# Performance work log

Measured on AMD Instinct MI355X. Metric: run time of the kernel, lower is better.

Reference implementation:

```python
import jax, jax.numpy as jnp
import numpy as np

B, N, D, W, IMG = 16384, 20, 64, 64, 2048
NUM_USERS, NUM_ITEMS, NUM_INGRE = 100000, 201000, 33001


def setup_inputs() -> dict:
    key = jax.random.key(0)
    ks = jax.random.split(key, 24)
    s = lambda *sh: 1.0 / np.sqrt(sh[0])
    inp = {
        'user_input': jax.random.randint(ks[0], (B,), 0, NUM_USERS),
        'item_input': jax.random.randint(ks[1], (B,), 0, NUM_ITEMS),
        'ingre_input': jax.random.randint(ks[2], (B, N), 0, NUM_INGRE),
        'image_input': jax.random.normal(ks[3], (B, IMG), dtype=jnp.float32),
        'ingre_num': jax.random.randint(ks[4], (B,), 1, N + 1),
        'user_emb': jax.random.normal(ks[5], (NUM_USERS, D), dtype=jnp.float32) * 0.01,
        'item_emb': jax.random.normal(ks[6], (NUM_ITEMS, D), dtype=jnp.float32) * 0.01,
        'ingre_emb': jax.random.normal(ks[7], (NUM_INGRE, D), dtype=jnp.float32) * 0.01,
        'W_image_w': jax.random.normal(ks[8], (IMG, D), dtype=jnp.float32) * s(IMG),
        'W_image_b': jnp.zeros((D,), jnp.float32),
        'b_image': jnp.zeros((1, D), jnp.float32),
        'W_concat_w': jax.random.normal(ks[9], (3 * D, D), dtype=jnp.float32) * s(3 * D),
        'W_concat_b': jnp.zeros((D,), jnp.float32),
        'b_concat': jnp.zeros((1, D), jnp.float32),
        'h_w': jax.random.normal(ks[10], (D, 1), dtype=jnp.float32) * s(D),
        'h_b': jnp.zeros((1,), jnp.float32),
        'W_att_ingre_w': jax.random.normal(ks[11], (3 * D, W), dtype=jnp.float32) * s(3 * D),
        'W_att_ingre_b': jnp.zeros((W,), jnp.float32),
        'b_att_ingre': jnp.zeros((1, W), jnp.float32),
        'v': jnp.ones((W, 1), jnp.float32),
        'W_att_com_w': jax.random.normal(ks[12], (2 * D, W), dtype=jnp.float32) * s(2 * D),
        'W_att_com_b': jnp.zeros((W,), jnp.float32),
        'b_att_com': jnp.zeros((1, W), jnp.float32),
        'v_c': jnp.ones((W, 1), jnp.float32),
    }
    return inp


def reference(user_input, item_input, ingre_input, image_input, ingre_num,
              user_emb, item_emb, ingre_emb,
              W_image_w, W_image_b, b_image,
              W_concat_w, W_concat_b, b_concat, h_w, h_b,
              W_att_ingre_w, W_att_ingre_b, b_att_ingre, v,
              W_att_com_w, W_att_com_b, b_att_com, v_c):
    b = user_input.shape[0]
    ue = user_emb[user_input]                       # [B, D]
    ie = item_emb[item_input]                       # [B, D]
    qe = ingre_emb[ingre_input]                     # [B, N, D]
    img = image_input @ W_image_w + W_image_b + b_image  # [B, D]

    # ---- ingredient-level attention ----
    n = qe.shape[1]
    tile_p = jnp.broadcast_to(ue[:, None, :], (b, n, ue.shape[-1]))
    tile_i = jnp.broadcast_to(img[:, None, :], (b, n, img.shape[-1]))
    concat_v = jnp.concatenate([qe, tile_p, tile_i], axis=2)     # [B, N, 3D]
    mlp = jnp.tanh(concat_v @ W_att_ingre_w + W_att_ingre_b + b_att_ingre[0])  # [B, N, W]
    A_ = (mlp @ v)[..., 0]                                        # [B, N]
    mask = (jnp.arange(n)[None, :] < ingre_num[:, None]).astype(A_.dtype)
    A_ = A_ * mask + (1.0 - mask) * (-1e12)
    A = jax.nn.softmax(A_, axis=1)[..., None]                     # [B, N, 1]
    ingre_att = jnp.sum(A * qe, axis=1)                           # [B, D]

    # ---- component-level attention (faithful to original cat+view order) ----
    cp = jnp.concatenate([
        jnp.concatenate([ue, ie], axis=1),
        jnp.concatenate([ue, ingre_att], axis=1),
        jnp.concatenate([ue, img], axis=1),
    ], axis=0)                                                    # [3B, 2D]
    ch = jnp.tanh(cp @ W_att_com_w + W_att_com_b + b_att_com[0])  # [3B, W]
    scores = (ch @ v_c).reshape(b, -1)                            # [B, 3] (row-major, as torch .view)
    Bw = jax.nn.softmax(scores, axis=1)[..., None]                # [B, 3, 1]
    ce = jnp.stack([ie, ingre_att, img], axis=1)                  # [B, 3, D]
    item_att = jnp.sum(Bw * ce, axis=1)                           # [B, D]

    # ---- prediction head ----
    uic = jnp.concatenate([ue, item_att, ue * item_att], axis=-1) # [B, 3D]
    hidden = jax.nn.relu(uic @ W_concat_w + W_concat_b + b_concat[0])
    out = hidden @ h_w + h_b                                      # [B, 1]
    return out
```

## Files before the change

kernel.cpp:

```cpp
#include <hip/hip_runtime.h>
#include <hip/hip_fp16.h>

#define BB 16384
#define NN 20
#define DD 64
#define IMGK 2048

using bf16x8 = __attribute__((ext_vector_type(8))) short;
using f32x4  = __attribute__((ext_vector_type(4))) float;

typedef __attribute__((address_space(1))) const unsigned int GUint;
typedef __attribute__((address_space(3))) unsigned int LUint;
__device__ __forceinline__ void gl_lds16(const void* g, void* l) {
  __builtin_amdgcn_global_load_lds((GUint*)g, (LUint*)l, 16, 0, 0);
}

__device__ __forceinline__ float waveReduceSum(float x) {
#pragma unroll
  for (int off = 32; off > 0; off >>= 1) x += __shfl_xor(x, off, 64);
  return x;
}

__device__ __forceinline__ float fast_tanh(float x) {
  float e = __expf(2.f * x);
  return 1.f - __fdividef(2.f, e + 1.f);
}

__device__ __forceinline__ short f2bf(float f) {
  union { float f; unsigned u; } c; c.f = f;
  unsigned r = c.u + 0x7fffu + ((c.u >> 16) & 1u);
  return (short)(r >> 16);
}
__device__ __forceinline__ float bf2f(short s) {
  union { unsigned u; float f; } c; c.u = ((unsigned)(unsigned short)s) << 16;
  return c.f;
}

__device__ __forceinline__ unsigned pack_hi(float a, float b) {
  unsigned ua = __float_as_uint(a), ub = __float_as_uint(b);
  return (ub & 0xffff0000u) | (ua >> 16);
}
__device__ __forceinline__ float trunc_bf(float a) {
  return __uint_as_float(__float_as_uint(a) & 0xffff0000u);
}

__global__ __launch_bounds__(256)
void prep_kernel(const float* __restrict__ Wimg, const float* __restrict__ W1,
                 short* __restrict__ Wf, short* __restrict__ W1f) {
  int i = blockIdx.x * 256 + threadIdx.x;
  if (i < 32768) {
    const int lane = i & 63;
    const int h = (i >> 6) & 1;
    const int tt = (i >> 7) & 3;
    const int ks = (i >> 9) & 1;
    const int kq = i >> 10;
    const int n = 16 * tt + (lane & 15);
    const int kb = kq * 64 + ks * 32 + (lane >> 4) * 8;
    union { short s[8]; bf16x8 v; } o;
#pragma unroll
    for (int j = 0; j < 8; ++j) {
      float f = Wimg[(size_t)(kb + j) * 64 + n];
      short hi = f2bf(f);
      o.s[j] = h == 0 ? hi : f2bf(f - bf2f(hi));
    }
    reinterpret_cast<bf16x8*>(Wf)[i] = o.v;
  } else if (i < 32768 + 1536) {
    const int j = i - 32768;
    const int lane = j & 63;
    const int wt = (j >> 6) & 3;
    const int ks = j >> 8;
    const int n = 16 * wt + (lane & 15);
    const int kb = ks * 32 + (lane >> 4) * 8;
    union { short s[8]; bf16x8 v; } o;
#pragma unroll
    for (int jj = 0; jj < 8; ++jj)
      o.s[jj] = f2bf(W1[(size_t)(kb + jj) * 64 + n]);
    reinterpret_cast<bf16x8*>(W1f)[j] = o.v;
  }
}

__global__ __launch_bounds__(256, 5)
void img_gemm_mfma(const float* __restrict__ img_in,
                   const short* __restrict__ Wf,
                   __half* __restrict__ pp) {
  __shared__ short wlds[8192];
  __shared__ float alds[4096];
  const int t = threadIdx.x;
  const int wave = t >> 6, lane = t & 63;
  const int lr = lane & 15, lk = lane >> 4;
  const int kq = blockIdx.x & 31, rgb = blockIdx.x >> 5;
  const int r0 = rgb * 64;
  __half* pout = pp + (size_t)kq * BB * 64;

  const short* wsrc = Wf + (size_t)kq * 8192;
#pragma unroll
  for (int i = 0; i < 4; ++i) {
    int j = i * 256 + t;
    gl_lds16(wsrc + j * 8, wlds + j * 8);
  }
#pragma unroll
  for (int i = 0; i < 4; ++i) {
    int j = i * 256 + t;
    int r = j >> 4, c = j & 15;
    int gc = (c ^ (r & 7)) * 4;
    gl_lds16(img_in + (size_t)(r0 + r) * IMGK + kq * 64 + gc, alds + j * 4);
  }
  asm volatile("s_waitcnt vmcnt(0)" ::: "memory");
  __syncthreads();

  const int arow = wave * 16 + lr;
  const int rx = arow & 7;
  float4 Af[2][2];
#pragma unroll
  for (int ks = 0; ks < 2; ++ks) {
    const int s0 = ks * 8 + lk * 2;
    Af[ks][0] = *reinterpret_cast<const float4*>(alds + arow * 64 + (s0 ^ rx) * 4);
    Af[ks][1] = *reinterpret_cast<const float4*>(alds + arow * 64 + ((s0 + 1) ^ rx) * 4);
  }
  const bf16x8* wp = reinterpret_cast<const bf16x8*>(wlds);
  f32x4 aHH[4], aER[4];
#pragma unroll
  for (int tt = 0; tt < 4; ++tt) {
    aHH[tt] = (f32x4){0.f, 0.f, 0.f, 0.f};
    aER[tt] = (f32x4){0.f, 0.f, 0.f, 0.f};
  }
#pragma unroll
  for (int ks = 0; ks < 2; ++ks) {
    float4 va = Af[ks][0], vb = Af[ks][1];
    union { unsigned u[4]; bf16x8 v; } hi, lo;
    hi.u[0] = pack_hi(va.x, va.y);
    hi.u[1] = pack_hi(va.z, va.w);
    hi.u[2] = pack_hi(vb.x, vb.y);
    hi.u[3] = pack_hi(vb.z, vb.w);
    lo.u[0] = pack_hi(va.x - trunc_bf(va.x), va.y - trunc_bf(va.y));
    lo.u[1] = pack_hi(va.z - trunc_bf(va.z), va.w - trunc_bf(va.w));
    lo.u[2] = pack_hi(vb.x - trunc_bf(vb.x), vb.y - trunc_bf(vb.y));
    lo.u[3] = pack_hi(vb.z - trunc_bf(vb.z), vb.w - trunc_bf(vb.w));
#pragma unroll
    for (int tt = 0; tt < 4; ++tt) {
      bf16x8 wh = wp[((ks * 4 + tt) * 2 + 0) * 64 + lane];
      bf16x8 wl = wp[((ks * 4 + tt) * 2 + 1) * 64 + lane];
      aHH[tt] = __builtin_amdgcn_mfma_f32_16x16x32_bf16(hi.v, wh, aHH[tt], 0, 0, 0);
      aER[tt] = __builtin_amdgcn_mfma_f32_16x16x32_bf16(hi.v, wl, aER[tt], 0, 0, 0);
      aER[tt] = __builtin_amdgcn_mfma_f32_16x16x32_bf16(lo.v, wh, aER[tt], 0, 0, 0);
    }
  }
#pragma unroll
  for (int tt = 0; tt < 4; ++tt)
#pragma unroll
    for (int r = 0; r < 4; ++r)
      pout[(size_t)(r0 + wave * 16 + 4 * lk + r) * 64 + 16 * tt + lr] =
          __float2half(aHH[tt][r] + aER[tt][r]);
}

__global__ __launch_bounds__(256, 3)
void mid_kernel(const int* __restrict__ user_input,
                const int* __restrict__ ingre_input,
                const int* __restrict__ ingre_num,
                const float* __restrict__ user_emb,
                const float* __restrict__ ingre_emb,
                const __half* __restrict__ pp,
                const float* __restrict__ Wb, const float* __restrict__ bimg,
                const short* __restrict__ W1f,
                const float* __restrict__ Wib, const float* __restrict__ bai,
                const float* __restrict__ v,
                float* __restrict__ ws_img,
                float* __restrict__ ws_ia) {
  __shared__ short wflds[12288];
  __shared__ short qe_s[4][32][88];
  __shared__ short ui_s[4][128];
  __shared__ float sc_s[4][32];
  const int t = threadIdx.x;
  const int wave = t >> 6, lane = t & 63;
  const int lr = lane & 15, lk = lane >> 4;
  const int b = blockIdx.x * 4 + wave;

  for (int i = t; i < 1536; i += 256)
    reinterpret_cast<bf16x8*>(wflds)[i] = reinterpret_cast<const bf16x8*>(W1f)[i];

  float qv[NN];
#pragma unroll
  for (int n = 0; n < NN; ++n) {
    const int gi = ingre_input[b * NN + n];
    qv[n] = ingre_emb[(size_t)gi * 64 + lane];
  }
  float s = Wb[lane] + bimg[lane];
#pragma unroll
  for (int kq = 0; kq < 32; ++kq)
    s += __half2float(pp[(size_t)kq * BB * 64 + (size_t)b * 64 + lane]);
  const int u = user_input[b];
  const float ue = user_emb[(size_t)u * 64 + lane];
  ws_img[(size_t)b * 64 + lane] = s;
  float vv[4], biasw[4];
#pragma unroll
  for (int wt = 0; wt < 4; ++wt) {
    vv[wt] = v[16 * wt + lr];
    biasw[wt] = Wib[16 * wt + lr] + bai[16 * wt + lr];
  }

#pragma unroll
  for (int n = 0; n < NN; ++n) qe_s[wave][n][lane] = f2bf(qv[n]);
#pragma unroll
  for (int n = NN; n < 32; ++n) qe_s[wave][n][lane] = 0;
  ui_s[wave][lane] = f2bf(ue);
  ui_s[wave][64 + lane] = f2bf(s);
  __syncthreads();

  bf16x8 aq0[2], aq1[2], au[4];
#pragma unroll
  for (int ks = 0; ks < 2; ++ks) {
    aq0[ks] = *reinterpret_cast<const bf16x8*>(&qe_s[wave][lr][ks * 32 + lk * 8]);
    aq1[ks] = *reinterpret_cast<const bf16x8*>(&qe_s[wave][16 + lr][ks * 32 + lk * 8]);
  }
#pragma unroll
  for (int ks = 0; ks < 4; ++ks)
    au[ks] = *reinterpret_cast<const bf16x8*>(&ui_s[wave][ks * 32 + lk * 8]);

  const bf16x8* wp = reinterpret_cast<const bf16x8*>(wflds);
  f32x4 accq[2][4], accb[4];
#pragma unroll
  for (int wt = 0; wt < 4; ++wt) {
    accq[0][wt] = (f32x4){0.f, 0.f, 0.f, 0.f};
    accq[1][wt] = (f32x4){0.f, 0.f, 0.f, 0.f};
    accb[wt] = (f32x4){0.f, 0.f, 0.f, 0.f};
  }
#pragma unroll
  for (int ks = 0; ks < 2; ++ks)
#pragma unroll
    for (int wt = 0; wt < 4; ++wt) {
      bf16x8 w = wp[(ks * 4 + wt) * 64 + lane];
      accq[0][wt] = __builtin_amdgcn_mfma_f32_16x16x32_bf16(aq0[ks], w, accq[0][wt], 0, 0, 0);
      accq[1][wt] = __builtin_amdgcn_mfma_f32_16x16x32_bf16(aq1[ks], w, accq[1][wt], 0, 0, 0);
    }
#pragma unroll
  for (int ks = 2; ks < 6; ++ks)
#pragma unroll
    for (int wt = 0; wt < 4; ++wt) {
      bf16x8 w = wp[(ks * 4 + wt) * 64 + lane];
      accb[wt] = __builtin_amdgcn_mfma_f32_16x16x32_bf16(au[ks - 2], w, accb[wt], 0, 0, 0);
    }
  float basew[4];
#pragma unroll
  for (int wt = 0; wt < 4; ++wt) basew[wt] = accb[wt][0] + biasw[wt];

  float sp[2][4];
#pragma unroll
  for (int nt = 0; nt < 2; ++nt)
#pragma unroll
    for (int r = 0; r < 4; ++r) {
      float sv = 0.f;
#pragma unroll
      for (int wt = 0; wt < 4; ++wt) {
        float x = accq[nt][wt][r] + basew[wt];
        sv = fmaf(fast_tanh(x), vv[wt], sv);
      }
      sp[nt][r] = sv;
    }
#pragma unroll
  for (int off = 1; off < 16; off <<= 1)
#pragma unroll
    for (int nt = 0; nt < 2; ++nt)
#pragma unroll
      for (int r = 0; r < 4; ++r) sp[nt][r] += __shfl_xor(sp[nt][r], off, 64);
  if (lr == 0) {
#pragma unroll
    for (int r = 0; r < 4; ++r) {
      sc_s[wave][4 * lk + r] = sp[0][r];
      sc_s[wave][16 + 4 * lk + r] = sp[1][r];
    }
  }
  asm volatile("s_waitcnt lgkmcnt(0)" ::: "memory");
  float scn[NN];
#pragma unroll
  for (int q = 0; q < 5; ++q) {
    float4 s4 = *reinterpret_cast<const float4*>(&sc_s[wave][4 * q]);
    scn[4 * q + 0] = s4.x; scn[4 * q + 1] = s4.y;
    scn[4 * q + 2] = s4.z; scn[4 * q + 3] = s4.w;
  }
  asm volatile("s_waitcnt lgkmcnt(0)" ::: "memory");
  const int num = ingre_num[b];
  float m = -3e38f;
#pragma unroll
  for (int n = 0; n < NN; ++n) {
    scn[n] = (n < num) ? scn[n] : -1e12f;
    m = fmaxf(m, scn[n]);
  }
  float ssum = 0.f;
#pragma unroll
  for (int n = 0; n < NN; ++n) {
    scn[n] = __expf(scn[n] - m);
    ssum += scn[n];
  }
  const float inv = __fdividef(1.f, ssum);
  float ia = 0.f;
#pragma unroll
  for (int n = 0; n < NN; ++n) ia = fmaf(scn[n], qv[n], ia);
  ws_ia[(size_t)b * 64 + lane] = ia * inv;
}

__global__ __launch_bounds__(256, 4)
void com_score_kernel(const int* __restrict__ user_input,
                      const int* __restrict__ item_input,
                      const float* __restrict__ user_emb,
                      const float* __restrict__ item_emb,
                      const float* __restrict__ Wc,
                      const float* __restrict__ Wcb,
                      const float* __restrict__ bat,
                      const float* __restrict__ vc,
                      const float* __restrict__ ws_img,
                      const float* __restrict__ ws_ia,
                      float* __restrict__ ws_flat) {
  __shared__ float Wclds[128 * 64];
  __shared__ float x_s[4][4][64];
  const int t = threadIdx.x;
  for (int i = t; i < 128 * 64 / 4; i += 256)
    reinterpret_cast<float4*>(Wclds)[i] = reinterpret_cast<const float4*>(Wc)[i];
  __syncthreads();
  const int wave = t >> 6, lane = t & 63;
  const float bb = Wcb[lane] + bat[lane];
  const float vcl = vc[lane];
  const int b0 = blockIdx.x * 16 + wave * 4;
#pragma unroll 1
  for (int bi = 0; bi < 4; ++bi) {
    const int b = b0 + bi;
    const int u = user_input[b];
    const int it = item_input[b];
    x_s[wave][0][lane] = user_emb[(size_t)u * 64 + lane];
    x_s[wave][1][lane] = item_emb[(size_t)it * 64 + lane];
    x_s[wave][2][lane] = ws_ia[(size_t)b * 64 + lane];
    x_s[wave][3][lane] = ws_img[(size_t)b * 64 + lane];
    asm volatile("s_waitcnt lgkmcnt(0)" ::: "memory");
    const float4* u4 = reinterpret_cast<const float4*>(&x_s[wave][0][0]);
    float up = 0.f;
#pragma unroll
    for (int d0 = 0; d0 < 16; ++d0) {
      float4 q = u4[d0];
      int d = d0 * 4;
      up = fmaf(q.x, Wclds[(d + 0) * 64 + lane],
           fmaf(q.y, Wclds[(d + 1) * 64 + lane],
           fmaf(q.z, Wclds[(d + 2) * 64 + lane],
           fmaf(q.w, Wclds[(d + 3) * 64 + lane], up))));
    }
    float sc[3];
#pragma unroll
    for (int c = 0; c < 3; ++c) {
      const float4* y4 = reinterpret_cast<const float4*>(&x_s[wave][1 + c][0]);
      float s = bb + up;
#pragma unroll
      for (int d0 = 0; d0 < 16; ++d0) {
        float4 q = y4[d0];
        int d = 64 + d0 * 4;
        s = fmaf(q.x, Wclds[(d + 0) * 64 + lane],
            fmaf(q.y, Wclds[(d + 1) * 64 + lane],
            fmaf(q.z, Wclds[(d + 2) * 64 + lane],
            fmaf(q.w, Wclds[(d + 3) * 64 + lane], s))));
      }
      sc[c] = waveReduceSum(fast_tanh(s) * vcl);
    }
    if (lane == 0) {
      ws_flat[b] = sc[0];
      ws_flat[BB + b] = sc[1];
      ws_flat[2 * BB + b] = sc[2];
    }
    asm volatile("s_waitcnt lgkmcnt(0)" ::: "memory");
  }
}

__global__ __launch_bounds__(256, 3)
void head_kernel(const int* __restrict__ user_input,
                 const int* __restrict__ item_input,
                 const float* __restrict__ user_emb,
                 const float* __restrict__ item_emb,
                 const float* __restrict__ Wcat,
                 const float* __restrict__ Wcatb,
                 const float* __restrict__ bcat,
                 const float* __restrict__ hw,
                 const float* __restrict__ hb,
                 const float* __restrict__ ws_img,
                 const float* __restrict__ ws_ia,
                 const float* __restrict__ ws_flat,
                 float* __restrict__ out) {
  __shared__ float Wlds[192 * 64];
  __shared__ float ue_s[4][64];
  __shared__ float itt_s[4][64];
  const int t = threadIdx.x;
  for (int i = t; i < 192 * 64 / 4; i += 256)
    reinterpret_cast<float4*>(Wlds)[i] = reinterpret_cast<const float4*>(Wcat)[i];
  __syncthreads();
  const int wave = t >> 6, lane = t & 63;
  const float bb = Wcatb[lane] + bcat[lane];
  const float hwl = hw[lane];
  const float hbv = hb[0];
  const int b0 = blockIdx.x * 16 + wave * 4;
#pragma unroll 1
  for (int bi = 0; bi < 4; ++bi) {
    const int b = b0 + bi;
    const float s0 = ws_flat[3 * b + 0];
    const float s1 = ws_flat[3 * b + 1];
    const float s2 = ws_flat[3 * b + 2];
    const float m = fmaxf(s0, fmaxf(s1, s2));
    const float e0 = __expf(s0 - m), e1 = __expf(s1 - m), e2 = __expf(s2 - m);
    const float inv = 1.0f / (e0 + e1 + e2);
    const int u = user_input[b];
    const int it = item_input[b];
    const float uev = user_emb[(size_t)u * 64 + lane];
    const float itt = (e0 * item_emb[(size_t)it * 64 + lane] +
                       e1 * ws_ia[(size_t)b * 64 + lane] +
                       e2 * ws_img[(size_t)b * 64 + lane]) * inv;
    ue_s[wave][lane] = uev;
    itt_s[wave][lane] = itt;
    asm volatile("s_waitcnt lgkmcnt(0)" ::: "memory");
    const float4* u4 = reinterpret_cast<const float4*>(&ue_s[wave][0]);
    const float4* i4 = reinterpret_cast<const float4*>(&itt_s[wave][0]);
    float h = bb;
#pragma unroll
    for (int d0 = 0; d0 < 16; ++d0) {
      float4 uu = u4[d0];
      float4 ii = i4[d0];
      int d = d0 * 4;
      h = fmaf(uu.x, Wlds[(d + 0) * 64 + lane], h);
      h = fmaf(ii.x, Wlds[(64 + d + 0) * 64 + lane], h);
      h = fmaf(uu.x * ii.x, Wlds[(128 + d + 0) * 64 + lane], h);
      h = fmaf(uu.y, Wlds[(d + 1) * 64 + lane], h);
      h = fmaf(ii.y, Wlds[(64 + d + 1) * 64 + lane], h);
      h = fmaf(uu.y * ii.y, Wlds[(128 + d + 1) * 64 + lane], h);
      h = fmaf(uu.z, Wlds[(d + 2) * 64 + lane], h);
      h = fmaf(ii.z, Wlds[(64 + d + 2) * 64 + lane], h);
      h = fmaf(uu.z * ii.z, Wlds[(128 + d + 2) * 64 + lane], h);
      h = fmaf(uu.w, Wlds[(d + 3) * 64 + lane], h);
      h = fmaf(ii.w, Wlds[(64 + d + 3) * 64 + lane], h);
      h = fmaf(uu.w * ii.w, Wlds[(128 + d + 3) * 64 + lane], h);
    }
    h = fmaxf(h, 0.f) * hwl;
    float o = waveReduceSum(h);
    if (lane == 0) out[b] = o + hbv;
    asm volatile("s_waitcnt lgkmcnt(0)" ::: "memory");
  }
}

extern "C" void kernel_launch(void* const* d_in, const int* in_sizes, int n_in,
                              void* d_out, int out_size, void* d_ws, size_t ws_size,
                              hipStream_t stream) {
  (void)in_sizes; (void)n_in; (void)out_size; (void)ws_size;
  const int* user_input = (const int*)d_in[0];
  const int* item_input = (const int*)d_in[1];
  const int* ingre_input = (const int*)d_in[2];
  const float* image_input = (const float*)d_in[3];
  const int* ingre_num = (const int*)d_in[4];
  const float* user_emb = (const float*)d_in[5];
  const float* item_emb = (const float*)d_in[6];
  const float* ingre_emb = (const float*)d_in[7];
  const float* W_image_w = (const float*)d_in[8];
  const float* W_image_b = (const float*)d_in[9];
  const float* b_image = (const float*)d_in[10];
  const float* W_concat_w = (const float*)d_in[11];
  const float* W_concat_b = (const float*)d_in[12];
  const float* b_concat = (const float*)d_in[13];
  const float* h_w = (const float*)d_in[14];
  const float* h_b = (const float*)d_in[15];
  const float* W_att_ingre_w = (const float*)d_in[16];
  const float* W_att_ingre_b = (const float*)d_in[17];
  const float* b_att_ingre = (const float*)d_in[18];
  const float* v = (const float*)d_in[19];
  const float* W_att_com_w = (const float*)d_in[20];
  const float* W_att_com_b = (const float*)d_in[21];
  const float* b_att_com = (const float*)d_in[22];
  const float* v_c = (const float*)d_in[23];

  float* ws = (float*)d_ws;
  float* ws_img = ws;
  float* ws_ia = ws + (size_t)BB * 64;
  float* ws_flat = ws + (size_t)2 * BB * 64;
  short* Wf = (short*)(ws + (size_t)2 * BB * 64 + 3 * BB);
  short* W1f = Wf + (size_t)32 * 8192;
  __half* pp = (__half*)(W1f + 12288);
  float* out = (float*)d_out;

  prep_kernel<<<(32768 + 1536 + 255) / 256, 256, 0, stream>>>(
      W_image_w, W_att_ingre_w, Wf, W1f);
  img_gemm_mfma<<<8192, 256, 0, stream>>>(image_input, Wf, pp);
  mid_kernel<<<BB / 4, 256, 0, stream>>>(user_input, ingre_input, ingre_num,
                                         user_emb, ingre_emb, pp,
                                         W_image_b, b_image, W1f,
                                         W_att_ingre_b, b_att_ingre, v,
                                         ws_img, ws_ia);
  com_score_kernel<<<BB / 16, 256, 0, stream>>>(user_input, item_input, user_emb, item_emb,
                                                W_att_com_w, W_att_com_b, b_att_com, v_c,
                                                ws_img, ws_ia, ws_flat);
  head_kernel<<<BB / 16, 256, 0, stream>>>(user_input, item_input, user_emb, item_emb,
                                           W_concat_w, W_concat_b, b_concat, h_w, h_b,
                                           ws_img, ws_ia, ws_flat, out);
}
```

Measured before the change: 144.6 us.

## Fuse component-attention scoring into mid kernel via MFMA and vectorize GEMM output stores

Removes the separate com_score kernel by computing the component-attention scores inside mid_kernel. It uses bf16 MFMA with a pre-packed W_att_com weight built in prep_kernel. This drops one launch and the re-reads of embeddings, image features and ingredient attention from global memory. The image GEMM epilogue now stages results through LDS so it can write coalesced 16-byte half stores instead of scattered 2-byte stores. The cost is bf16 rounding in the score projection, extra register and LDS use in mid_kernel, and mostly-idle MFMA rows.

```diff
diff --git a/kernel.cpp b/kernel.cpp
--- a/kernel.cpp
+++ b/kernel.cpp
@@ -46,7 +46,9 @@
 
 __global__ __launch_bounds__(256)
 void prep_kernel(const float* __restrict__ Wimg, const float* __restrict__ W1,
-                 short* __restrict__ Wf, short* __restrict__ W1f) {
+                 const float* __restrict__ Wc,
+                 short* __restrict__ Wf, short* __restrict__ W1f,
+                 short* __restrict__ Wcf) {
   int i = blockIdx.x * 256 + threadIdx.x;
   if (i < 32768) {
     const int lane = i & 63;
@@ -76,6 +78,18 @@
     for (int jj = 0; jj < 8; ++jj)
       o.s[jj] = f2bf(W1[(size_t)(kb + jj) * 64 + n]);
     reinterpret_cast<bf16x8*>(W1f)[j] = o.v;
+  } else if (i < 32768 + 1536 + 1024) {
+    const int j = i - 32768 - 1536;
+    const int lane = j & 63;
+    const int wt = (j >> 6) & 3;
+    const int ks = j >> 8;
+    const int n = 16 * wt + (lane & 15);
+    const int kb = ks * 32 + (lane >> 4) * 8;
+    union { short s[8]; bf16x8 v; } o;
+#pragma unroll
+    for (int jj = 0; jj < 8; ++jj)
+      o.s[jj] = f2bf(Wc[(size_t)(kb + jj) * 64 + n]);
+    reinterpret_cast<bf16x8*>(Wcf)[j] = o.v;
   }
 }
 
@@ -149,26 +163,46 @@
   for (int tt = 0; tt < 4; ++tt)
 #pragma unroll
     for (int r = 0; r < 4; ++r)
-      pout[(size_t)(r0 + wave * 16 + 4 * lk + r) * 64 + 16 * tt + lr] =
-          __float2half(aHH[tt][r] + aER[tt][r]);
+      alds[(size_t)(wave * 16 + 4 * lk + r) * 64 + 16 * tt + lr] = aHH[tt][r] + aER[tt][r];
+  asm volatile("s_waitcnt lgkmcnt(0)" ::: "memory");
+  {
+    const int row_l = lane >> 2, colq = (lane & 3) * 16;
+    const float* src = alds + (size_t)(wave * 16 + row_l) * 64 + colq;
+    union { __half h[8]; int4 v; } o1, o2;
+#pragma unroll
+    for (int j = 0; j < 8; ++j) {
+      o1.h[j] = __float2half(src[j]);
+      o2.h[j] = __float2half(src[8 + j]);
+    }
+    __half* dst = pout + (size_t)(r0 + wave * 16 + row_l) * 64 + colq;
+    *reinterpret_cast<int4*>(dst) = o1.v;
+    *reinterpret_cast<int4*>(dst + 8) = o2.v;
+  }
 }
 
 __global__ __launch_bounds__(256, 3)
 void mid_kernel(const int* __restrict__ user_input,
+                const int* __restrict__ item_input,
                 const int* __restrict__ ingre_input,
                 const int* __restrict__ ingre_num,
                 const float* __restrict__ user_emb,
+                const float* __restrict__ item_emb,
                 const float* __restrict__ ingre_emb,
                 const __half* __restrict__ pp,
                 const float* __restrict__ Wb, const float* __restrict__ bimg,
                 const short* __restrict__ W1f,
                 const float* __restrict__ Wib, const float* __restrict__ bai,
                 const float* __restrict__ v,
+                const short* __restrict__ Wcf,
+                const float* __restrict__ Wcb, const float* __restrict__ bac,
+                const float* __restrict__ vc,
                 float* __restrict__ ws_img,
-                float* __restrict__ ws_ia) {
+                float* __restrict__ ws_ia,
+                float* __restrict__ ws_flat) {
   __shared__ short wflds[12288];
   __shared__ short qe_s[4][32][88];
-  __shared__ short ui_s[4][128];
+  __shared__ short ui_s[4][256];
+  __shared__ float P4_s[4][4][64];
   __shared__ float sc_s[4][32];
   const int t = threadIdx.x;
   const int wave = t >> 6, lane = t & 63;
@@ -189,7 +223,9 @@
   for (int kq = 0; kq < 32; ++kq)
     s += __half2float(pp[(size_t)kq * BB * 64 + (size_t)b * 64 + lane]);
   const int u = user_input[b];
+  const int it = item_input[b];
   const float ue = user_emb[(size_t)u * 64 + lane];
+  const float iev = item_emb[(size_t)it * 64 + lane];
   ws_img[(size_t)b * 64 + lane] = s;
   float vv[4], biasw[4];
 #pragma unroll
@@ -197,6 +233,8 @@
     vv[wt] = v[16 * wt + lr];
     biasw[wt] = Wib[16 * wt + lr] + bai[16 * wt + lr];
   }
+  const float bbc = Wcb[lane] + bac[lane];
+  const float vcl = vc[lane];
 
 #pragma unroll
   for (int n = 0; n < NN; ++n) qe_s[wave][n][lane] = f2bf(qv[n]);
@@ -204,6 +242,7 @@
   for (int n = NN; n < 32; ++n) qe_s[wave][n][lane] = 0;
   ui_s[wave][lane] = f2bf(ue);
   ui_s[wave][64 + lane] = f2bf(s);
+  ui_s[wave][128 + lane] = f2bf(iev);
   __syncthreads();
 
   bf16x8 aq0[2], aq1[2], au[4];
@@ -295,74 +334,54 @@
   float ia = 0.f;
 #pragma unroll
   for (int n = 0; n < NN; ++n) ia = fmaf(scn[n], qv[n], ia);
-  ws_ia[(size_t)b * 64 + lane] = ia * inv;
-}
-
-__global__ __launch_bounds__(256, 4)
-void com_score_kernel(const int* __restrict__ user_input,
-                      const int* __restrict__ item_input,
-                      const float* __restrict__ user_emb,
-                      const float* __restrict__ item_emb,
-                      const float* __restrict__ Wc,
-                      const float* __restrict__ Wcb,
-                      const float* __restrict__ bat,
-                      const float* __restrict__ vc,
-                      const float* __restrict__ ws_img,
-                      const float* __restrict__ ws_ia,
-                      float* __restrict__ ws_flat) {
-  __shared__ float Wclds[128 * 64];
-  __shared__ float x_s[4][4][64];
-  const int t = threadIdx.x;
-  for (int i = t; i < 128 * 64 / 4; i += 256)
-    reinterpret_cast<float4*>(Wclds)[i] = reinterpret_cast<const float4*>(Wc)[i];
-  __syncthreads();
-  const int wave = t >> 6, lane = t & 63;
-  const float bb = Wcb[lane] + bat[lane];
-  const float vcl = vc[lane];
-  const int b0 = blockIdx.x * 16 + wave * 4;
-#pragma unroll 1
-  for (int bi = 0; bi < 4; ++bi) {
-    const int b = b0 + bi;
-    const int u = user_input[b];
-    const int it = item_input[b];
-    x_s[wave][0][lane] = user_emb[(size_t)u * 64 + lane];
-    x_s[wave][1][lane] = item_emb[(size_t)it * 64 + lane];
-    x_s[wave][2][lane] = ws_ia[(size_t)b * 64 + lane];
-    x_s[wave][3][lane] = ws_img[(size_t)b * 64 + lane];
-    asm volatile("s_waitcnt lgkmcnt(0)" ::: "memory");
-    const float4* u4 = reinterpret_cast<const float4*>(&x_s[wave][0][0]);
-    float up = 0.f;
-#pragma unroll
-    for (int d0 = 0; d0 < 16; ++d0) {
-      float4 q = u4[d0];
-      int d = d0 * 4;
-      up = fmaf(q.x, Wclds[(d + 0) * 64 + lane],
-           fmaf(q.y, Wclds[(d + 1) * 64 + lane],
-           fmaf(q.z, Wclds[(d + 2) * 64 + lane],
-           fmaf(q.w, Wclds[(d + 3) * 64 + lane], up))));
-    }
-    float sc[3];
-#pragma unroll
-    for (int c = 0; c < 3; ++c) {
-      const float4* y4 = reinterpret_cast<const float4*>(&x_s[wave][1 + c][0]);
-      float s = bb + up;
-#pragma unroll
-      for (int d0 = 0; d0 < 16; ++d0) {
-        float4 q = y4[d0];
-        int d = 64 + d0 * 4;
-        s = fmaf(q.x, Wclds[(d + 0) * 64 + lane],
-            fmaf(q.y, Wclds[(d + 1) * 64 + lane],
-            fmaf(q.z, Wclds[(d + 2) * 64 + lane],
-            fmaf(q.w, Wclds[(d + 3) * 64 + lane], s))));
-      }
-      sc[c] = waveReduceSum(fast_tanh(s) * vcl);
-    }
-    if (lane == 0) {
-      ws_flat[b] = sc[0];
-      ws_flat[BB + b] = sc[1];
-      ws_flat[2 * BB + b] = sc[2];
-    }
-    asm volatile("s_waitcnt lgkmcnt(0)" ::: "memory");
+  ia *= inv;
+  ws_ia[(size_t)b * 64 + lane] = ia;
+
+  ui_s[wave][192 + lane] = f2bf(ia);
+  asm volatile("s_waitcnt lgkmcnt(0)" ::: "memory");
+  const bf16x8 zerov = (bf16x8){0, 0, 0, 0, 0, 0, 0, 0};
+  f32x4 accU[4], accY[4];
+#pragma unroll
+  for (int wt = 0; wt < 4; ++wt) {
+    accU[wt] = (f32x4){0.f, 0.f, 0.f, 0.f};
+    accY[wt] = (f32x4){0.f, 0.f, 0.f, 0.f};
+  }
+  const int yoff = (lr == 0) ? 128 : (lr == 1) ? 192 : 64;
+#pragma unroll
+  for (int ks = 0; ks < 2; ++ks) {
+    bf16x8 aU = (lr == 0)
+        ? *reinterpret_cast<const bf16x8*>(&ui_s[wave][ks * 32 + lk * 8]) : zerov;
+    bf16x8 aY = (lr < 3)
+        ? *reinterpret_cast<const bf16x8*>(&ui_s[wave][yoff + ks * 32 + lk * 8]) : zerov;
+#pragma unroll
+    for (int wt = 0; wt < 4; ++wt) {
+      bf16x8 wU = *reinterpret_cast<const bf16x8*>(Wcf + ((ks * 4 + wt) * 64 + lane) * 8);
+      bf16x8 wY = *reinterpret_cast<const bf16x8*>(Wcf + (((ks + 2) * 4 + wt) * 64 + lane) * 8);
+      accU[wt] = __builtin_amdgcn_mfma_f32_16x16x32_bf16(aU, wU, accU[wt], 0, 0, 0);
+      accY[wt] = __builtin_amdgcn_mfma_f32_16x16x32_bf16(aY, wY, accY[wt], 0, 0, 0);
+    }
+  }
+  if (lk == 0) {
+#pragma unroll
+    for (int wt = 0; wt < 4; ++wt) {
+      P4_s[wave][0][wt * 16 + lr] = accU[wt][0];
+      P4_s[wave][1][wt * 16 + lr] = accY[wt][0];
+      P4_s[wave][2][wt * 16 + lr] = accY[wt][1];
+      P4_s[wave][3][wt * 16 + lr] = accY[wt][2];
+    }
+  }
+  asm volatile("s_waitcnt lgkmcnt(0)" ::: "memory");
+  const float su = P4_s[wave][0][lane] + bbc;
+  float sc3[3];
+#pragma unroll
+  for (int c = 0; c < 3; ++c) {
+    float x = su + P4_s[wave][1 + c][lane];
+    sc3[c] = waveReduceSum(fast_tanh(x) * vcl);
+  }
+  if (lane == 0) {
+    ws_flat[b] = sc3[0];
+    ws_flat[BB + b] = sc3[1];
+    ws_flat[2 * BB + b] = sc3[2];
   }
 }
 
@@ -473,20 +492,19 @@
   float* ws_flat = ws + (size_t)2 * BB * 64;
   short* Wf = (short*)(ws + (size_t)2 * BB * 64 + 3 * BB);
   short* W1f = Wf + (size_t)32 * 8192;
-  __half* pp = (__half*)(W1f + 12288);
+  short* Wcf = W1f + 12288;
+  __half* pp = (__half*)(Wcf + 8192);
   float* out = (float*)d_out;
 
-  prep_kernel<<<(32768 + 1536 + 255) / 256, 256, 0, stream>>>(
-      W_image_w, W_att_ingre_w, Wf, W1f);
+  prep_kernel<<<(32768 + 1536 + 1024 + 255) / 256, 256, 0, stream>>>(
+      W_image_w, W_att_ingre_w, W_att_com_w, Wf, W1f, Wcf);
   img_gemm_mfma<<<8192, 256, 0, stream>>>(image_input, Wf, pp);
-  mid_kernel<<<BB / 4, 256, 0, stream>>>(user_input, ingre_input, ingre_num,
-                                         user_emb, ingre_emb, pp,
+  mid_kernel<<<BB / 4, 256, 0, stream>>>(user_input, item_input, ingre_input, ingre_num,
+                                         user_emb, item_emb, ingre_emb, pp,
                                          W_image_b, b_image, W1f,
                                          W_att_ingre_b, b_att_ingre, v,
-                                         ws_img, ws_ia);
-  com_score_kernel<<<BB / 16, 256, 0, stream>>>(user_input, item_input, user_emb, item_emb,
-                                                W_att_com_w, W_att_com_b, b_att_com, v_c,
-                                                ws_img, ws_ia, ws_flat);
+                                         Wcf, W_att_com_b, b_att_com, v_c,
+                                         ws_img, ws_ia, ws_flat);
   head_kernel<<<BB / 16, 256, 0, stream>>>(user_input, item_input, user_emb, item_emb,
                                            W_concat_w, W_concat_b, b_concat, h_w, h_b,
                                            ws_img, ws_ia, ws_flat, out);
```

Measured after the change: 127.1 us. 12.1% less time.
